# Performance work log

Hardware: AMD Instinct MI355X
Metric: run time of the kernel (lower is better)

The kernel has to match this reference:

```python
import jax, jax.numpy as jnp
import numpy as np

N = 100000   # nodes
E = 1600000  # edges (avg degree 16)
F_IN = 128
H = 128
C = 16


def setup_inputs() -> dict:
    key = jax.random.key(0)
    ks = jax.random.split(key, 13)
    s = 1.0 / np.sqrt(H)
    return {
        "x": jax.random.normal(ks[0], (N, F_IN), jnp.float32),
        "edge_index": jax.random.randint(ks[1], (2, E), 0, N, jnp.int32),
        "edge_weight": jax.random.uniform(ks[2], (E,), jnp.float32),
        "W1": jax.random.normal(ks[3], (F_IN, H), jnp.float32) * s,
        "b1": jnp.zeros((H,), jnp.float32),
        "W2": jax.random.normal(ks[4], (H, H), jnp.float32) * s,
        "b2": jnp.zeros((H,), jnp.float32),
        "Wg": jax.random.normal(ks[5], (H, H), jnp.float32) * s,
        "att_src": jax.random.normal(ks[6], (H,), jnp.float32) * s,
        "att_dst": jax.random.normal(ks[7], (H,), jnp.float32) * s,
        "bg": jnp.zeros((H,), jnp.float32),
        "Wc": jax.random.normal(ks[8], (H, C), jnp.float32) * s,
        "bc": jnp.zeros((C,), jnp.float32),
    }


def reference(x, edge_index, edge_weight, W1, b1, W2, b2, Wg, att_src, att_dst, bg, Wc, bc):
    n = x.shape[0]
    loop = jnp.arange(n, dtype=edge_index.dtype)
    src = jnp.concatenate([edge_index[0], loop])   # self loops (PyG default)
    dst = jnp.concatenate([edge_index[1], loop])
    ew = jnp.concatenate([edge_weight, jnp.ones((n,), x.dtype)])  # loop weight 1

    # GCN normalization: D^{-1/2} A D^{-1/2}, degree on dst with edge weights
    deg = jax.ops.segment_sum(ew, dst, num_segments=n)
    dinv = jnp.where(deg > 0, jax.lax.rsqrt(deg), 0.0)
    norm = dinv[src] * ew * dinv[dst]              # [E+N]

    def gcn(h, W, b):
        h = h @ W                                   # [N,H]
        agg = jax.ops.segment_sum(h[src] * norm[:, None], dst, num_segments=n)
        return agg + b

    h = jax.nn.relu(gcn(x, W1, b1))
    h = jax.nn.relu(gcn(h, W2, b2))                 # dropout inert in eval

    # GATConv, heads=1
    g = h @ Wg                                      # [N,H]
    a = jax.nn.leaky_relu((g @ att_src)[src] + (g @ att_dst)[dst], 0.2)
    amax = jax.ops.segment_max(a, dst, num_segments=n)
    ex = jnp.exp(a - amax[dst])
    denom = jax.ops.segment_sum(ex, dst, num_segments=n)
    alpha = ex / denom[dst]                         # edge softmax per dst
    out = jax.ops.segment_sum(g[src] * alpha[:, None], dst, num_segments=n) + bg
    out = jax.nn.relu(out)
    return out @ Wc + bc
```

## Files before the change

### kernel.cpp

```cpp
#include <hip/hip_runtime.h>
#include <hip/hip_fp16.h>

#define FIN 128
#define HD 128
#define COUT 16

#define SLOT_CAP 48
#define CS_BLOCKS 512
#define CB_SHIFT 9
#define CB_SIZE 512
#define CAP_B 10240
#define GMK_CELLS 64
#define NBINS 49
#define SBUF_CAP 3136

typedef _Float16 half8 __attribute__((ext_vector_type(8)));
typedef float floatx4 __attribute__((ext_vector_type(4)));

__device__ __forceinline__ float lrelu02(float x) { return x > 0.f ? x : 0.2f * x; }

union U4H8 { uint4 q; __half2 h2[4]; };
union UQH8 { uint4 q; half8 h; _Float16 e[8]; };

__device__ __forceinline__ void h8f(const uint4 q, float* f) {
    U4H8 u; u.q = q;
    float2 a0 = __half22float2(u.h2[0]);
    float2 a1 = __half22float2(u.h2[1]);
    float2 a2 = __half22float2(u.h2[2]);
    float2 a3 = __half22float2(u.h2[3]);
    f[0] = a0.x; f[1] = a0.y; f[2] = a1.x; f[3] = a1.y;
    f[4] = a2.x; f[5] = a2.y; f[6] = a3.x; f[7] = a3.y;
}

__device__ __forceinline__ unsigned fkey(float f) {
    unsigned u = __float_as_uint(f);
    return (u & 0x80000000u) ? ~u : (u | 0x80000000u);
}
__device__ __forceinline__ float funkey(unsigned k) {
    return (k & 0x80000000u) ? __uint_as_float(k ^ 0x80000000u)
                             : __uint_as_float(~k);
}

__global__ void k_setup(const float* __restrict__ W1, const float* __restrict__ W2,
                        const float* __restrict__ Wg, __half* __restrict__ w1z,
                        __half* __restrict__ w2z, __half* __restrict__ wgz,
                        int* __restrict__ cur, unsigned* __restrict__ gmk,
                        int* __restrict__ hist) {
    int b = blockIdx.x;
    if (b < 24) {
        const float* W = (b < 8) ? W1 : (b < 16) ? W2 : Wg;
        __half* outp   = (b < 8) ? w1z : (b < 16) ? w2z : wgz;
        int t = (b & 7) * 256 + threadIdx.x;
        int lane = t & 63;
        int kc = (t >> 6) & 3;
        int nt = t >> 8;
        int kbase = kc * 32 + (lane >> 4) * 8;
        int col = nt * 16 + (lane & 15);
        UQH8 u;
#pragma unroll
        for (int j = 0; j < 8; j++)
            u.e[j] = (_Float16)W[(kbase + j) * 128 + col];
        ((uint4*)outp)[t] = u.q;
    } else {
        cur[threadIdx.x] = 0;
        if (threadIdx.x < 64) hist[threadIdx.x] = 0;
        for (int i = threadIdx.x; i < GMK_CELLS * 16; i += 256)
            gmk[i] = 0u;
    }
}

__device__ __forceinline__
void gemm_body_f32(int blk, const float* __restrict__ A, const __half* __restrict__ Wz,
                   __half* __restrict__ Out, int n) {
    int wave = threadIdx.x >> 6;
    int lane = threadIdx.x & 63;
    int m0 = blk * 64 + wave * 16;
    if (m0 >= n) return;
    int m = lane & 15;
    int quad = lane >> 4;

    half8 a[4];
#pragma unroll
    for (int kc = 0; kc < 4; kc++) {
        const float* p = &A[(size_t)(m0 + m) * 128 + kc * 32 + quad * 8];
        float4 f0 = *(const float4*)p;
        float4 f1 = *(const float4*)(p + 4);
        UQH8 u;
        u.e[0] = (_Float16)f0.x; u.e[1] = (_Float16)f0.y;
        u.e[2] = (_Float16)f0.z; u.e[3] = (_Float16)f0.w;
        u.e[4] = (_Float16)f1.x; u.e[5] = (_Float16)f1.y;
        u.e[6] = (_Float16)f1.z; u.e[7] = (_Float16)f1.w;
        a[kc] = u.h;
    }

    floatx4 acc[8];
#pragma unroll
    for (int nt = 0; nt < 8; nt++) acc[nt] = (floatx4){0.f, 0.f, 0.f, 0.f};

    const uint4* Wv = (const uint4*)Wz;
#pragma unroll
    for (int kc = 0; kc < 4; kc++) {
#pragma unroll
        for (int nt = 0; nt < 8; nt++) {
            UQH8 u;
            u.q = Wv[(nt * 4 + kc) * 64 + lane];
            acc[nt] = __builtin_amdgcn_mfma_f32_16x16x32_f16(a[kc], u.h, acc[nt], 0, 0, 0);
        }
    }
#pragma unroll
    for (int nt = 0; nt < 8; nt++) {
#pragma unroll
        for (int reg = 0; reg < 4; reg++) {
            Out[(size_t)(m0 + quad * 4 + reg) * 128 + nt * 16 + m] =
                __float2half(acc[nt][reg]);
        }
    }
}

__launch_bounds__(256)
__global__ void k_csc_gemm(const int* __restrict__ src, const int* __restrict__ dst,
                           const float* __restrict__ ew, int* __restrict__ cur,
                           int2* __restrict__ coarseBuf, int e,
                           const float* __restrict__ x, const __half* __restrict__ w1z,
                           __half* __restrict__ buf0, int n) {
    __shared__ int2 sbuf[SBUF_CAP];
    __shared__ unsigned short sbufb[SBUF_CAP];
    __shared__ int lcnt[256], lofs[256], lpos[256], lbase[256];
    if ((int)blockIdx.x < CS_BLOCKS) {
        int tid = threadIdx.x;
        int chunk = (e + CS_BLOCKS - 1) / CS_BLOCKS;
        int s0 = blockIdx.x * chunk;
        int s1 = min(s0 + chunk, e);
        for (int t0 = s0; t0 < s1; t0 += SBUF_CAP) {
            int t1 = min(t0 + SBUF_CAP, s1);
            lcnt[tid] = 0; lpos[tid] = 0;
            __syncthreads();
            for (int i = t0 + tid; i < t1; i += 256)
                atomicAdd(&lcnt[dst[i] >> CB_SHIFT], 1);
            __syncthreads();
            lofs[tid] = lcnt[tid];
            __syncthreads();
            for (int d = 1; d < 256; d <<= 1) {
                int v = (tid >= d) ? lofs[tid - d] : 0;
                __syncthreads();
                lofs[tid] += v;
                __syncthreads();
            }
            if (lcnt[tid] > 0) lbase[tid] = atomicAdd(&cur[tid], lcnt[tid]);
            __syncthreads();
            for (int i = t0 + tid; i < t1; i += 256) {
                int d = dst[i];
                int b = d >> CB_SHIFT;
                int p = (lofs[b] - lcnt[b]) + atomicAdd(&lpos[b], 1);
                sbuf[p] = make_int2(((d & (CB_SIZE - 1)) << 17) | src[i],
                                    __float_as_int(ew[i]));
                sbufb[p] = (unsigned short)b;
            }
            __syncthreads();
            int total = t1 - t0;
            for (int t = tid; t < total; t += 256) {
                int b = sbufb[t];
                int local = t - (lofs[b] - lcnt[b]);
                int gpos = lbase[b] + local;
                if (gpos < CAP_B)
                    coarseBuf[(size_t)b * CAP_B + gpos] = sbuf[t];
            }
            __syncthreads();
        }
    } else {
        gemm_body_f32(blockIdx.x - CS_BLOCKS, x, w1z, buf0, n);
    }
}

__launch_bounds__(512)
__global__ void k_fine(const int2* __restrict__ coarseBuf, const int* __restrict__ cur,
                       int2* __restrict__ slots, int* __restrict__ cnt,
                       float* __restrict__ dinv, int* __restrict__ hist, int n) {
    __shared__ int lcnt[CB_SIZE];
    __shared__ float lsum[CB_SIZE];
    __shared__ int lhist[NBINS];
    int b = blockIdx.x;
    int tid = threadIdx.x;
    if (tid < CB_SIZE) { lcnt[tid] = 0; lsum[tid] = 0.f; }
    if (tid < NBINS) lhist[tid] = 0;
    __syncthreads();
    int ecnt = min(cur[b], CAP_B);
    size_t e0 = (size_t)b * CAP_B;
    for (int e = tid; e < ecnt; e += 512) {
        int2 it = coarseBuf[e0 + e];
        int dl = (it.x >> 17) & (CB_SIZE - 1);
        int srcn = it.x & 0x1FFFF;
        int pos = atomicAdd(&lcnt[dl], 1);
        atomicAdd(&lsum[dl], __int_as_float(it.y));
        if (pos < SLOT_CAP) {
            int node = (b << CB_SHIFT) + dl;
            slots[(size_t)node * SLOT_CAP + pos] = make_int2(srcn, it.y);
        }
    }
    __syncthreads();
    if (tid < CB_SIZE) {
        int node = (b << CB_SHIFT) + tid;
        if (node < n) {
            int c = min(lcnt[tid], SLOT_CAP);
            cnt[node] = c;
            dinv[node] = rsqrtf(1.0f + lsum[tid]);
            atomicAdd(&lhist[c], 1);
        }
    }
    __syncthreads();
    if (tid < NBINS && lhist[tid] > 0) atomicAdd(&hist[tid], lhist[tid]);
}

__global__ void k_prefix(const int* __restrict__ hist, int* __restrict__ binCur) {
    if (threadIdx.x == 0) {
        int acc = 0;
        for (int c = 0; c < NBINS; c++) { binCur[c] = acc; acc += hist[c]; }
    }
}

__launch_bounds__(512)
__global__ void k_permscatter(const int* __restrict__ cnt, int* __restrict__ binCur,
                              int* __restrict__ perm, int n) {
    __shared__ int lh[NBINS], lb[NBINS], lp[NBINS];
    int tid = threadIdx.x;
    if (tid < NBINS) { lh[tid] = 0; lp[tid] = 0; }
    __syncthreads();
    int node = blockIdx.x * 512 + tid;
    int c = -1;
    if (node < n) { c = cnt[node]; atomicAdd(&lh[c], 1); }
    __syncthreads();
    if (tid < NBINS && lh[tid] > 0) lb[tid] = atomicAdd(&binCur[tid], lh[tid]);
    __syncthreads();
    if (node < n) {
        int pos = lb[c] + atomicAdd(&lp[c], 1);
        perm[pos] = node;
    }
}

__device__ __forceinline__
void gather_body(int node, int lane, const int* __restrict__ cnt,
                 const int2* __restrict__ slots, const uint4* __restrict__ tv,
                 const float* __restrict__ dinv, const float* __restrict__ b,
                 float* __restrict__ fout) {
    float dd = dinv[node];
    float sw = dd * dd;
    float acc[8];
    {
        uint4 q = tv[(size_t)node * 16 + lane];
        float f[8]; h8f(q, f);
#pragma unroll
        for (int j = 0; j < 8; j++) acc[j] = f[j] * sw;
    }
    int r0 = (int)((size_t)node * SLOT_CAP);
    int r1 = r0 + cnt[node];
    int e = r0;
    for (; e + 8 <= r1; e += 8) {
        int2 c[8];
        float dv[8];
        uint4 v[8];
#pragma unroll
        for (int j = 0; j < 8; j++) c[j] = slots[e + j];
#pragma unroll
        for (int j = 0; j < 8; j++) dv[j] = dinv[c[j].x];
#pragma unroll
        for (int j = 0; j < 8; j++) v[j] = tv[(size_t)c[j].x * 16 + lane];
#pragma unroll
        for (int j = 0; j < 8; j++) {
            float w = dv[j] * __int_as_float(c[j].y) * dd;
            float f[8]; h8f(v[j], f);
#pragma unroll
            for (int k = 0; k < 8; k++) acc[k] = fmaf(f[k], w, acc[k]);
        }
    }
    for (; e + 2 <= r1; e += 2) {
        int2 c0 = slots[e], c1 = slots[e + 1];
        float dv0 = dinv[c0.x], dv1 = dinv[c1.x];
        uint4 v0 = tv[(size_t)c0.x * 16 + lane];
        uint4 v1 = tv[(size_t)c1.x * 16 + lane];
        float w0 = dv0 * __int_as_float(c0.y) * dd;
        float w1 = dv1 * __int_as_float(c1.y) * dd;
        float f0[8], f1[8]; h8f(v0, f0); h8f(v1, f1);
#pragma unroll
        for (int k = 0; k < 8; k++) acc[k] = fmaf(f0[k], w0, acc[k]);
#pragma unroll
        for (int k = 0; k < 8; k++) acc[k] = fmaf(f1[k], w1, acc[k]);
    }
    if (e < r1) {
        int2 c = slots[e];
        uint4 v = tv[(size_t)c.x * 16 + lane];
        float w = dinv[c.x] * __int_as_float(c.y) * dd;
        float f[8]; h8f(v, f);
#pragma unroll
        for (int k = 0; k < 8; k++) acc[k] = fmaf(f[k], w, acc[k]);
    }
    const float4* b4 = (const float4*)b;
    float4 bb0 = b4[lane * 2], bb1 = b4[lane * 2 + 1];
    fout[0] = fmaxf(acc[0] + bb0.x, 0.f);
    fout[1] = fmaxf(acc[1] + bb0.y, 0.f);
    fout[2] = fmaxf(acc[2] + bb0.z, 0.f);
    fout[3] = fmaxf(acc[3] + bb0.w, 0.f);
    fout[4] = fmaxf(acc[4] + bb1.x, 0.f);
    fout[5] = fmaxf(acc[5] + bb1.y, 0.f);
    fout[6] = fmaxf(acc[6] + bb1.z, 0.f);
    fout[7] = fmaxf(acc[7] + bb1.w, 0.f);
}

template <bool ATTN>
__launch_bounds__(256)
__global__ void k_gather_gemm(const int* __restrict__ cnt, const int2* __restrict__ slots,
                              const __half* __restrict__ t, const float* __restrict__ dinv,
                              const float* __restrict__ b, const __half* __restrict__ Wz,
                              __half* __restrict__ Out, const int* __restrict__ perm,
                              const float* __restrict__ attS, const float* __restrict__ attD,
                              float* __restrict__ as_, float* __restrict__ ad_,
                              unsigned* __restrict__ gmaxKey, int n) {
    __shared__ __half stage[16][136];
    __shared__ float redS[4][16], redD[4][16];
    int tid = threadIdx.x;
    int nl = tid >> 4;
    int lane16 = tid & 15;
    int idx16 = blockIdx.x * 16 + nl;
    int node = (idx16 < n) ? perm[idx16] : -1;

    if (node >= 0) {
        float f[8];
        gather_body(node, lane16, cnt, slots, (const uint4*)t, dinv, b, f);
        UQH8 u;
#pragma unroll
        for (int j = 0; j < 8; j++) u.e[j] = (_Float16)f[j];
        *(uint4*)&stage[nl][lane16 * 8] = u.q;
    } else {
        UQH8 u;
#pragma unroll
        for (int j = 0; j < 8; j++) u.e[j] = (_Float16)0.f;
        *(uint4*)&stage[nl][lane16 * 8] = u.q;
    }
    __syncthreads();

    int wave = tid >> 6;
    int lane = tid & 63;
    int m = lane & 15;
    int quad = lane >> 4;
    int m0 = blockIdx.x * 16;

    half8 a[4];
#pragma unroll
    for (int kc = 0; kc < 4; kc++)
        a[kc] = *(const half8*)&stage[m][kc * 32 + quad * 8];

    floatx4 acc[2];
    acc[0] = (floatx4){0.f, 0.f, 0.f, 0.f};
    acc[1] = (floatx4){0.f, 0.f, 0.f, 0.f};
    const uint4* Wv = (const uint4*)Wz;
#pragma unroll
    for (int t2 = 0; t2 < 2; t2++) {
        int nt = wave * 2 + t2;
#pragma unroll
        for (int kc = 0; kc < 4; kc++) {
            UQH8 u;
            u.q = Wv[(nt * 4 + kc) * 64 + lane];
            acc[t2] = __builtin_amdgcn_mfma_f32_16x16x32_f16(a[kc], u.h, acc[t2], 0, 0, 0);
        }
    }
#pragma unroll
    for (int reg = 0; reg < 4; reg++) {
        int row = m0 + quad * 4 + reg;
        if (row < n) {
            int prow = perm[row];
#pragma unroll
            for (int t2 = 0; t2 < 2; t2++) {
                int col = (wave * 2 + t2) * 16 + m;
                Out[(size_t)prow * 128 + col] = __float2half(acc[t2][reg]);
            }
        }
    }

    if (ATTN) {
        float sv0 = attS[(wave * 2 + 0) * 16 + m], sv1 = attS[(wave * 2 + 1) * 16 + m];
        float dv0 = attD[(wave * 2 + 0) * 16 + m], dv1 = attD[(wave * 2 + 1) * 16 + m];
#pragma unroll
        for (int reg = 0; reg < 4; reg++) {
            float s = acc[0][reg] * sv0 + acc[1][reg] * sv1;
            float d = acc[0][reg] * dv0 + acc[1][reg] * dv1;
#pragma unroll
            for (int k = 8; k >= 1; k >>= 1) {
                s += __shfl_xor(s, k, 64);
                d += __shfl_xor(d, k, 64);
            }
            if (m == 0) {
                redS[wave][quad * 4 + reg] = s;
                redD[wave][quad * 4 + reg] = d;
            }
        }
        __syncthreads();
        if (tid < 16) {
            int nd = m0 + tid;
            unsigned key = 0u;
            if (nd < n) {
                float sv = redS[0][tid] + redS[1][tid] + redS[2][tid] + redS[3][tid];
                float dv = redD[0][tid] + redD[1][tid] + redD[2][tid] + redD[3][tid];
                int pn = perm[nd];
                as_[pn] = sv;
                ad_[pn] = dv;
                key = fkey(sv);
            }
#pragma unroll
            for (int k = 8; k >= 1; k >>= 1) {
                unsigned o = (unsigned)__shfl_xor((int)key, k, 64);
                key = key > o ? key : o;
            }
            if (tid == 0)
                atomicMax(&gmaxKey[(blockIdx.x & (GMK_CELLS - 1)) << 4], key);
        }
    }
}

__launch_bounds__(256)
__global__ void k_gat_final(const int* __restrict__ cnt, const int2* __restrict__ slots,
                            const __half* __restrict__ g, const float* __restrict__ as_,
                            const float* __restrict__ ad_,
                            const unsigned* __restrict__ gmaxKey,
                            const int* __restrict__ perm,
                            const float* __restrict__ bg,
                            const float* __restrict__ Wc, const float* __restrict__ bc,
                            float* __restrict__ out, int n) {
    __shared__ float Wcs[128 * 16];
    __shared__ float bcs[16];
    __shared__ float stage[16][136];
    __shared__ float gmaxS;
    int tid = threadIdx.x;
    for (int i = tid; i < 128 * 16; i += 256) Wcs[i] = Wc[i];
    if (tid < 16) bcs[tid] = bc[tid];

    if (tid < 64) {
        unsigned k = gmaxKey[tid << 4];
#pragma unroll
        for (int d = 32; d >= 1; d >>= 1) {
            unsigned o = (unsigned)__shfl_xor((int)k, d, 64);
            k = k > o ? k : o;
        }
        if (tid == 0) gmaxS = funkey(k);
    }
    __syncthreads();
    float gmax = gmaxS;

    int idx = blockIdx.x * 256 + tid;
    int lidx = idx >> 4;
    int node = (lidx < n) ? perm[lidx] : -1;
    int lane = idx & 15;
    int nl = tid >> 4;

    if (node >= 0) {
        int r0 = (int)((size_t)node * SLOT_CAP);
        int r1 = r0 + cnt[node];
        float ad_d = ad_[node];
        float c = lrelu02(gmax + ad_d);
        const uint4* gv = (const uint4*)g;
        float ex = __expf(lrelu02(as_[node] + ad_d) - c);
        float den = ex;
        float acc[8];
        {
            uint4 q = gv[(size_t)node * 16 + lane];
            float f[8]; h8f(q, f);
#pragma unroll
            for (int j = 0; j < 8; j++) acc[j] = ex * f[j];
        }
        int e = r0;
        for (; e + 8 <= r1; e += 8) {
            int s[8];
            float av[8];
            uint4 u[8];
#pragma unroll
            for (int j = 0; j < 8; j++) s[j] = slots[e + j].x;
#pragma unroll
            for (int j = 0; j < 8; j++) av[j] = as_[s[j]];
#pragma unroll
            for (int j = 0; j < 8; j++) u[j] = gv[(size_t)s[j] * 16 + lane];
#pragma unroll
            for (int j = 0; j < 8; j++) {
                float w = __expf(lrelu02(av[j] + ad_d) - c);
                den += w;
                float f[8]; h8f(u[j], f);
#pragma unroll
                for (int k = 0; k < 8; k++) acc[k] = fmaf(f[k], w, acc[k]);
            }
        }
        for (; e + 2 <= r1; e += 2) {
            int s0 = slots[e].x, s1 = slots[e + 1].x;
            uint4 u0 = gv[(size_t)s0 * 16 + lane];
            uint4 u1 = gv[(size_t)s1 * 16 + lane];
            float w0 = __expf(lrelu02(as_[s0] + ad_d) - c);
            float w1 = __expf(lrelu02(as_[s1] + ad_d) - c);
            den += w0 + w1;
            float f0[8], f1[8]; h8f(u0, f0); h8f(u1, f1);
#pragma unroll
            for (int k = 0; k < 8; k++) acc[k] = fmaf(f0[k], w0, acc[k]);
#pragma unroll
            for (int k = 0; k < 8; k++) acc[k] = fmaf(f1[k], w1, acc[k]);
        }
        if (e < r1) {
            int s = slots[e].x;
            uint4 u = gv[(size_t)s * 16 + lane];
            float w = __expf(lrelu02(as_[s] + ad_d) - c);
            den += w;
            float f[8]; h8f(u, f);
#pragma unroll
            for (int k = 0; k < 8; k++) acc[k] = fmaf(f[k], w, acc[k]);
        }
        float inv = 1.0f / den;
        const float4* bg4 = (const float4*)bg;
        float4 b0 = bg4[lane * 2], b1 = bg4[lane * 2 + 1];
        float* sp = &stage[nl][lane * 8];
        sp[0] = fmaxf(acc[0] * inv + b0.x, 0.f);
        sp[1] = fmaxf(acc[1] * inv + b0.y, 0.f);
        sp[2] = fmaxf(acc[2] * inv + b0.z, 0.f);
        sp[3] = fmaxf(acc[3] * inv + b0.w, 0.f);
        sp[4] = fmaxf(acc[4] * inv + b1.x, 0.f);
        sp[5] = fmaxf(acc[5] * inv + b1.y, 0.f);
        sp[6] = fmaxf(acc[6] * inv + b1.z, 0.f);
        sp[7] = fmaxf(acc[7] * inv + b1.w, 0.f);
    }
    __syncthreads();
    int nl2 = tid >> 4;
    int col = tid & 15;
    int oidx = blockIdx.x * 16 + nl2;
    if (oidx >= n) return;
    int onode = perm[oidx];
    float accp = bcs[col];
    const float* sp = stage[nl2];
#pragma unroll 8
    for (int k = 0; k < 128; k++)
        accp = fmaf(sp[k], Wcs[k * 16 + col], accp);
    out[(size_t)onode * 16 + col] = accp;
}

extern "C" void kernel_launch(void* const* d_in, const int* in_sizes, int n_in,
                              void* d_out, int out_size, void* d_ws, size_t ws_size,
                              hipStream_t stream) {
    const float* x      = (const float*)d_in[0];
    const int*   eidx   = (const int*)d_in[1];
    const float* ew     = (const float*)d_in[2];
    const float* W1     = (const float*)d_in[3];
    const float* b1     = (const float*)d_in[4];
    const float* W2     = (const float*)d_in[5];
    const float* b2     = (const float*)d_in[6];
    const float* Wg     = (const float*)d_in[7];
    const float* attS   = (const float*)d_in[8];
    const float* attD   = (const float*)d_in[9];
    const float* bg     = (const float*)d_in[10];
    const float* Wc     = (const float*)d_in[11];
    const float* bc     = (const float*)d_in[12];

    const int N = in_sizes[0] / FIN;
    const int E = in_sizes[2];
    const int* src = eidx;
    const int* dst = eidx + E;
    const int NB = (N + CB_SIZE - 1) >> CB_SHIFT;

    char* base = (char*)d_ws;
    size_t off = 0;
    auto carve = [&](size_t bytes) {
        char* q = base + off;
        off = (off + bytes + 255) & ~(size_t)255;
        return (void*)q;
    };
    int*    cnt       = (int*)carve((size_t)N * 4);
    int*    cur       = (int*)carve(256 * 4);
    unsigned* gmk     = (unsigned*)carve((size_t)GMK_CELLS * 16 * 4);
    int*    hist      = (int*)carve(64 * 4);
    int*    binCur    = (int*)carve(64 * 4);
    int*    perm      = (int*)carve((size_t)N * 4);
    int2*   coarseBuf = (int2*)carve((size_t)NB * CAP_B * 8);
    int2*   slots     = (int2*)carve((size_t)N * SLOT_CAP * 8);
    float*  dinv      = (float*)carve((size_t)N * 4);
    float*  as_       = (float*)carve((size_t)N * 4);
    float*  ad_       = (float*)carve((size_t)N * 4);
    __half* w1z       = (__half*)carve((size_t)128 * 128 * 2);
    __half* w2z       = (__half*)carve((size_t)128 * 128 * 2);
    __half* wgz       = (__half*)carve((size_t)128 * 128 * 2);
    __half* buf0      = (__half*)carve((size_t)N * 128 * 2);
    __half* buf1      = (__half*)carve((size_t)N * 128 * 2);

    const int B = 256;
    dim3 blk(B);
    int fusedGrid = (N + 15) / 16;
    int gemmGrid = (N + 63) / 64;

    k_setup<<<25, blk, 0, stream>>>(W1, W2, Wg, w1z, w2z, wgz, cur, gmk, hist);
    k_csc_gemm<<<CS_BLOCKS + gemmGrid, blk, 0, stream>>>(src, dst, ew, cur, coarseBuf, E,
                                                         x, w1z, buf0, N);
    k_fine<<<NB, dim3(512), 0, stream>>>(coarseBuf, cur, slots, cnt, dinv, hist, N);
    k_prefix<<<1, dim3(64), 0, stream>>>(hist, binCur);
    k_permscatter<<<NB, dim3(512), 0, stream>>>(cnt, binCur, perm, N);

    k_gather_gemm<false><<<fusedGrid, blk, 0, stream>>>(cnt, slots, buf0, dinv, b1, w2z,
                                                        buf1, perm, nullptr, nullptr,
                                                        nullptr, nullptr, nullptr, N);
    k_gather_gemm<true><<<fusedGrid, blk, 0, stream>>>(cnt, slots, buf1, dinv, b2, wgz,
                                                       buf0, perm, attS, attD, as_, ad_,
                                                       gmk, N);
    k_gat_final<<<fusedGrid, blk, 0, stream>>>(cnt, slots, buf0, as_, ad_, gmk, perm, bg,
                                               Wc, bc, (float*)d_out, N);
}
```

Before: 406.0 us.

## Split layer-1 GEMM across CSC and fine kernels; fold prefix into last block

The first-layer X·W1 GEMM is split: the first ~40% of rows stay in the coarse-scatter kernel and the rest run as extra blocks of k_fine, so the GEMM work overlaps with both graph-build phases. The separate single-thread k_prefix launch is removed; the last k_fine block to finish, detected with a done-counter atomic in the hist array, computes binCur. This is meant to cut one kernel launch and balance work between the two kernels. It adds a scalar tail path for partial rows and relies on the atomic completion counter and fences being correct.

```diff
diff --git a/kernel.cpp b/kernel.cpp
--- a/kernel.cpp
+++ b/kernel.cpp
@@ -13,6 +13,7 @@
 #define GMK_CELLS 64
 #define NBINS 49
 #define SBUF_CAP 3136
+#define DONE_SLOT 50
 
 typedef _Float16 half8 __attribute__((ext_vector_type(8)));
 typedef float floatx4 __attribute__((ext_vector_type(4)));
@@ -70,11 +71,8 @@
 }
 
 __device__ __forceinline__
-void gemm_body_f32(int blk, const float* __restrict__ A, const __half* __restrict__ Wz,
-                   __half* __restrict__ Out, int n) {
-    int wave = threadIdx.x >> 6;
-    int lane = threadIdx.x & 63;
-    int m0 = blk * 64 + wave * 16;
+void gemm_rows16(int m0, const float* __restrict__ A, const __half* __restrict__ Wz,
+                 __half* __restrict__ Out, int lane, int n) {
     if (m0 >= n) return;
     int m = lane & 15;
     int quad = lane >> 4;
@@ -108,21 +106,23 @@
         }
     }
 #pragma unroll
-    for (int nt = 0; nt < 8; nt++) {
-#pragma unroll
-        for (int reg = 0; reg < 4; reg++) {
-            Out[(size_t)(m0 + quad * 4 + reg) * 128 + nt * 16 + m] =
-                __float2half(acc[nt][reg]);
-        }
-    }
-}
+    for (int reg = 0; reg < 4; reg++) {
+        int row = m0 + quad * 4 + reg;
+        if (row < n) {
+#pragma unroll
+            for (int nt = 0; nt < 8; nt++)
+                Out[(size_t)row * 128 + nt * 16 + m] = __float2half(acc[nt][reg]);
+        }
+    }
+}
+
 
 __launch_bounds__(256)
 __global__ void k_csc_gemm(const int* __restrict__ src, const int* __restrict__ dst,
                            const float* __restrict__ ew, int* __restrict__ cur,
                            int2* __restrict__ coarseBuf, int e,
                            const float* __restrict__ x, const __half* __restrict__ w1z,
-                           __half* __restrict__ buf0, int n) {
+                           __half* __restrict__ buf0, int nGemm) {
     __shared__ int2 sbuf[SBUF_CAP];
     __shared__ unsigned short sbufb[SBUF_CAP];
     __shared__ int lcnt[256], lofs[256], lpos[256], lbase[256];
@@ -168,17 +168,54 @@
             __syncthreads();
         }
     } else {
-        gemm_body_f32(blockIdx.x - CS_BLOCKS, x, w1z, buf0, n);
+        int blk = blockIdx.x - CS_BLOCKS;
+        int wave = threadIdx.x >> 6;
+        int lane = threadIdx.x & 63;
+        gemm_rows16(blk * 64 + wave * 16, x, w1z, buf0, lane, nGemm);
     }
 }
 
 __launch_bounds__(512)
 __global__ void k_fine(const int2* __restrict__ coarseBuf, const int* __restrict__ cur,
                        int2* __restrict__ slots, int* __restrict__ cnt,
-                       float* __restrict__ dinv, int* __restrict__ hist, int n) {
+                       float* __restrict__ dinv, int* __restrict__ hist,
+                       int* __restrict__ binCur, int NBv, int RA, int n,
+                       const float* __restrict__ x, const __half* __restrict__ w1z,
+                       __half* __restrict__ buf0) {
     __shared__ int lcnt[CB_SIZE];
     __shared__ float lsum[CB_SIZE];
     __shared__ int lhist[NBINS];
+    if ((int)blockIdx.x >= NBv) {
+        int fb = blockIdx.x - NBv;
+        int wave = threadIdx.x >> 6;
+        int lane = threadIdx.x & 63;
+        int m0 = RA + fb * 128 + wave * 16;
+        if (m0 + 15 < n) {
+            gemm_rows16(m0, x, w1z, buf0, lane, n);
+        } else if (m0 < n) {
+            int m = lane & 15;
+            if (m0 + m < n) {
+                for (int row = m0; row < n; row++) {
+                    int col = threadIdx.x & 127;
+                    int half_ = threadIdx.x >> 7;
+                    if (row % 4 != half_ && false) {}
+                    if ((threadIdx.x >> 7) == (row & 3)) {
+                        float acc = 0.f;
+                        for (int k = 0; k < 128; k++) {
+                            int nt = col >> 4, c16 = col & 15;
+                            int kc = k >> 5, kr = k & 31;
+                            int lane2 = (kr >> 3) * 16 + c16;
+                            int j = kr & 7;
+                            const __half* wp = w1z + ((size_t)(nt * 4 + kc) * 64 + lane2) * 8 + j;
+                            acc += x[(size_t)row * 128 + k] * __half2float(*wp);
+                        }
+                        buf0[(size_t)row * 128 + col] = __float2half(acc);
+                    }
+                }
+            }
+        }
+        return;
+    }
     int b = blockIdx.x;
     int tid = threadIdx.x;
     if (tid < CB_SIZE) { lcnt[tid] = 0; lsum[tid] = 0.f; }
@@ -209,12 +246,17 @@
     }
     __syncthreads();
     if (tid < NBINS && lhist[tid] > 0) atomicAdd(&hist[tid], lhist[tid]);
-}
-
-__global__ void k_prefix(const int* __restrict__ hist, int* __restrict__ binCur) {
-    if (threadIdx.x == 0) {
-        int acc = 0;
-        for (int c = 0; c < NBINS; c++) { binCur[c] = acc; acc += hist[c]; }
+    __syncthreads();
+    if (tid == 0) {
+        __threadfence();
+        if (atomicAdd(&hist[DONE_SLOT], 1) == NBv - 1) {
+            int acc = 0;
+            for (int c2 = 0; c2 < NBINS; c2++) {
+                int h = atomicAdd(&hist[c2], 0);
+                binCur[c2] = acc;
+                acc += h;
+            }
+        }
     }
 }
 
@@ -556,6 +598,11 @@
     const int* src = eidx;
     const int* dst = eidx + E;
     const int NB = (N + CB_SIZE - 1) >> CB_SHIFT;
+
+    int RA = (N * 2 / 5) & ~63;
+    if (RA > N) RA = N & ~63;
+    int gemmGridA = RA / 64;
+    int fineGemmGrid = (N > RA) ? (N - RA + 127) / 128 : 0;
 
     char* base = (char*)d_ws;
     size_t off = 0;
@@ -584,13 +631,13 @@
     const int B = 256;
     dim3 blk(B);
     int fusedGrid = (N + 15) / 16;
-    int gemmGrid = (N + 63) / 64;
 
     k_setup<<<25, blk, 0, stream>>>(W1, W2, Wg, w1z, w2z, wgz, cur, gmk, hist);
-    k_csc_gemm<<<CS_BLOCKS + gemmGrid, blk, 0, stream>>>(src, dst, ew, cur, coarseBuf, E,
-                                                         x, w1z, buf0, N);
-    k_fine<<<NB, dim3(512), 0, stream>>>(coarseBuf, cur, slots, cnt, dinv, hist, N);
-    k_prefix<<<1, dim3(64), 0, stream>>>(hist, binCur);
+    k_csc_gemm<<<CS_BLOCKS + gemmGridA, blk, 0, stream>>>(src, dst, ew, cur, coarseBuf, E,
+                                                          x, w1z, buf0, RA);
+    k_fine<<<NB + fineGemmGrid, dim3(512), 0, stream>>>(coarseBuf, cur, slots, cnt,
+                                                        dinv, hist, binCur, NB, RA, N,
+                                                        x, w1z, buf0);
     k_permscatter<<<NB, dim3(512), 0, stream>>>(cnt, binCur, perm, N);
 
     k_gather_gemm<false><<<fusedGrid, blk, 0, stream>>>(cnt, slots, buf0, dinv, b1, w2z,
```

New measurement: 426.1 us. 1.05x slower.
